# Performance work log

Measured on AMD Instinct MI355X. Metric: run time of the kernel, lower is better.

The kernel has to match this reference:

```python
import jax, jax.numpy as jnp
import numpy as np

N = 100000      # nodes
E = 1600000     # edges
F_IN, HID, OUT = 128, 64, 40


def gcn_conv(x, edge_index, W, b, num_nodes):
    """PyG GCNConv: linear transform, add self-loops, symmetric deg^-1/2 norm, scatter-add."""
    h = x @ W  # [N, F_out]
    loops = jnp.arange(num_nodes, dtype=edge_index.dtype)
    row = jnp.concatenate([edge_index[0], loops])  # source
    col = jnp.concatenate([edge_index[1], loops])  # target
    ones = jnp.ones(row.shape[0], dtype=h.dtype)
    deg = jax.ops.segment_sum(ones, col, num_segments=num_nodes)  # in-degree incl. self-loop
    dinv = jnp.where(deg > 0, jax.lax.rsqrt(deg), 0.0)
    norm = dinv[row] * dinv[col]                      # [E+N]
    msg = h[row] * norm[:, None]                      # gather + scale
    out = jax.ops.segment_sum(msg, col, num_segments=num_nodes)  # scatter-add
    return out + b


def setup_inputs() -> dict:
    key = jax.random.key(0)
    k = jax.random.split(key, 6)
    x = jax.random.normal(k[0], (N, F_IN), dtype=jnp.float32)
    edge_index = jax.random.randint(k[1], (2, E), 0, N, dtype=jnp.int32)
    W1 = jax.random.normal(k[2], (F_IN, HID), dtype=jnp.float32) / np.sqrt(F_IN)
    b1 = jnp.zeros((HID,), dtype=jnp.float32)
    W2 = jax.random.normal(k[3], (HID, OUT), dtype=jnp.float32) / np.sqrt(HID)
    b2 = jnp.zeros((OUT,), dtype=jnp.float32)
    return {"x": x, "edge_index": edge_index, "W1": W1, "b1": b1, "W2": W2, "b2": b2}


def reference(x, edge_index, W1, b1, W2, b2):
    h = gcn_conv(x, edge_index, W1, b1, N)
    h = jax.nn.relu(h)
    # dropout is identity in eval mode (F.dropout(training=False))
    h = gcn_conv(h, edge_index, W2, b2, N)
    return jax.nn.log_softmax(h, axis=1)
```

## Files before the change

kernel.cpp:

```cpp
#include <hip/hip_runtime.h>
#include <math.h>

#define NN 100000
#define NE 1600000
#define F_IN 128
#define HID 64
#define OUTF 40
#define NBKT 391
#define BCAPB 5120
#define TILE 16384
#define NTILES 98

typedef unsigned short u16;

__device__ __forceinline__ u16 f2bf(float f) {
    unsigned int x = __float_as_uint(f);
    return (u16)((x + 0x7fffu + ((x >> 16) & 1u)) >> 16);
}

__device__ __forceinline__ void add8(const int4 v, float* acc) {
    acc[0] += __uint_as_float(((unsigned)v.x) << 16);
    acc[1] += __uint_as_float(v.x & 0xffff0000u);
    acc[2] += __uint_as_float(((unsigned)v.y) << 16);
    acc[3] += __uint_as_float(v.y & 0xffff0000u);
    acc[4] += __uint_as_float(((unsigned)v.z) << 16);
    acc[5] += __uint_as_float(v.z & 0xffff0000u);
    acc[6] += __uint_as_float(((unsigned)v.w) << 16);
    acc[7] += __uint_as_float(v.w & 0xffff0000u);
}

__global__ void k_zero(int* bcnt) {
    int i = threadIdx.x;
    if (i < NBKT) bcnt[i] = 0;
}

__launch_bounds__(1024)
__global__ void k_bucket(const int* __restrict__ ei, int* __restrict__ bcnt,
                         int* __restrict__ bkt) {
    __shared__ int hist[NBKT], goff[NBKT], cur[NBKT];
    __shared__ int ss[512];
    __shared__ int stage[TILE];
    int t = threadIdx.x;
    int e0 = blockIdx.x * TILE;
    int ecnt = min(TILE, NE - e0);
    if (t < NBKT) hist[t] = 0;
    __syncthreads();
    for (int i = t; i < ecnt; i += 1024)
        atomicAdd(&hist[ei[NE + e0 + i] >> 8], 1);
    __syncthreads();
    if (t < 512) ss[t] = (t < NBKT) ? hist[t] : 0;
    __syncthreads();
    for (int o = 1; o < 512; o <<= 1) {
        int add = (t >= o && t < 512) ? ss[t - o] : 0;
        __syncthreads();
        if (t < 512) ss[t] += add;
        __syncthreads();
    }
    if (t < NBKT) cur[t] = ss[t] - hist[t];
    if (t < NBKT) goff[t] = atomicAdd(&bcnt[t], hist[t]);
    __syncthreads();
    for (int i = t; i < ecnt; i += 1024) {
        int c = ei[NE + e0 + i];
        int r = ei[e0 + i];
        int pos = atomicAdd(&cur[c >> 8], 1);
        stage[pos] = ((c & 255) << 17) | r;
    }
    __syncthreads();
    int wv = t >> 6, ln = t & 63;
    for (int b = wv; b < NBKT; b += 16) {
        int cnt = hist[b];
        int lo = cur[b] - cnt;
        int gb = b * BCAPB + goff[b];
        for (int i = ln; i < cnt; i += 64)
            bkt[gb + i] = stage[lo + i];
    }
}

__global__ void k_scanb(int* __restrict__ bcnt, int* __restrict__ bboff) {
    __shared__ int s[512];
    int t = threadIdx.x;
    int v = (t < NBKT) ? bcnt[t] : 0;
    s[t] = v;
    __syncthreads();
    for (int o = 1; o < 512; o <<= 1) {
        int add = (t >= o) ? s[t - o] : 0;
        __syncthreads();
        s[t] += add;
        __syncthreads();
    }
    if (t < NBKT) bboff[t] = s[t] - v;
}

__launch_bounds__(256)
__global__ void k_csr(const int* __restrict__ bcnt, const int* __restrict__ bboff,
                      const int* __restrict__ bkt, float* __restrict__ dinv,
                      int* __restrict__ cursor, int* __restrict__ eidx) {
    __shared__ int hist[256], loff[256], cur[256], sscan[256];
    __shared__ int stage[BCAPB];
    int t = threadIdx.x;
    int b = blockIdx.x;
    int cnt = bcnt[b];
    int base = bboff[b];
    const int* bp = bkt + b * BCAPB;
    hist[t] = 0;
    __syncthreads();
    for (int i = t; i < cnt; i += 256)
        atomicAdd(&hist[bp[i] >> 17], 1);
    __syncthreads();
    int n = b * 256 + t;
    int d = hist[t];
    if (n < NN) dinv[n] = rsqrtf((float)(d + 1));
    sscan[t] = d;
    __syncthreads();
    for (int o = 1; o < 256; o <<= 1) {
        int add = (t >= o) ? sscan[t - o] : 0;
        __syncthreads();
        sscan[t] += add;
        __syncthreads();
    }
    loff[t] = sscan[t] - d;
    cur[t] = 0;
    if (n < NN) cursor[n] = base + sscan[t];
    __syncthreads();
    for (int i = t; i < cnt; i += 256) {
        int v = bp[i];
        int pos = loff[v >> 17] + atomicAdd(&cur[v >> 17], 1);
        stage[pos] = v & 0x1FFFF;
    }
    __syncthreads();
    for (int i = t; i < cnt; i += 256)
        eidx[base + i] = stage[i];
}

__launch_bounds__(256)
__global__ void k_gemm1(const float* __restrict__ x, const float* __restrict__ W1,
                        const float* __restrict__ dinv, u16* __restrict__ h1) {
    __shared__ float Xs[64][132];
    __shared__ float Ws[128][64];
    int t = threadIdx.x;
    int row0 = blockIdx.x * 64;

#pragma unroll
    for (int i = 0; i < 8; i++) {
        int idx4 = t + 256 * i;
        float4 v = ((const float4*)W1)[idx4];
        int k = idx4 >> 4;
        int c4 = (idx4 & 15) << 2;
        *(float4*)&Ws[k][c4] = v;
    }
#pragma unroll
    for (int i = 0; i < 8; i++) {
        int idx4 = t + 256 * i;
        int r = idx4 >> 5;
        int k4 = (idx4 & 31) << 2;
        int gr = row0 + r;
        if (gr >= NN) gr = NN - 1;
        float4 v = *(const float4*)&x[gr * F_IN + k4];
        *(float4*)&Xs[r][k4] = v;
    }
    __syncthreads();

    int tx = t & 15, ty = t >> 4;
    int cb = tx << 2, rb = ty << 2;
    float acc[4][4] = {};
#pragma unroll 2
    for (int k = 0; k < F_IN; k += 4) {
        float4 xv[4], wv[4];
#pragma unroll
        for (int i = 0; i < 4; i++) xv[i] = *(const float4*)&Xs[rb + i][k];
#pragma unroll
        for (int kk = 0; kk < 4; kk++) wv[kk] = *(const float4*)&Ws[k + kk][cb];
#pragma unroll
        for (int i = 0; i < 4; i++) {
            const float* xp = (const float*)&xv[i];
#pragma unroll
            for (int kk = 0; kk < 4; kk++) {
                acc[i][0] += xp[kk] * wv[kk].x;
                acc[i][1] += xp[kk] * wv[kk].y;
                acc[i][2] += xp[kk] * wv[kk].z;
                acc[i][3] += xp[kk] * wv[kk].w;
            }
        }
    }
#pragma unroll
    for (int i = 0; i < 4; i++) {
        int gr = row0 + rb + i;
        if (gr < NN) {
            float dn = dinv[gr];
            ushort4 o;
            o.x = f2bf(acc[i][0] * dn); o.y = f2bf(acc[i][1] * dn);
            o.z = f2bf(acc[i][2] * dn); o.w = f2bf(acc[i][3] * dn);
            *(ushort4*)&h1[(size_t)gr * HID + cb] = o;
        }
    }
}

template <bool RELU_BIAS>
__global__ void k_agg(const int* __restrict__ cursor, const int* __restrict__ eidx,
                      const float* __restrict__ dinv, const u16* __restrict__ h,
                      const float* __restrict__ bias, u16* __restrict__ outp) {
    int lane = threadIdx.x & 63;
    int wid = (blockIdx.x * blockDim.x + threadIdx.x) >> 6;
    int half = lane >> 5;
    int li = lane & 31;
    int n = wid * 2 + half;
    int eg = (lane >> 3) & 3;
    int fo = (lane & 7) * 8;
    int hbase = lane & 32;
    int end = cursor[n];
    int start = (n == 0) ? 0 : cursor[n - 1];
    int deg = end - start;
    int degw = max(deg, __shfl_xor(deg, 32, 64));

    float acc[8] = {}, acc2[8] = {};
    if (eg == 0) {
        int4 hv = *(const int4*)&h[n * HID + fo];
        add8(hv, acc);
    }
    for (int c0 = 0; c0 < degw; c0 += 32) {
        int m = min(32, deg - c0);
        int mw = min(32, degw - c0);
        int sidx = (li < m) ? eidx[start + c0 + li] : 0;
        int kmax = (mw + 3) >> 2;
        int k = 0;
        for (; k + 2 <= kmax; k += 2) {
            int e0 = eg + (k << 2), e1 = e0 + 4;
            int s0 = __shfl(sidx, hbase + e0, 64);
            int s1 = __shfl(sidx, hbase + e1, 64);
            if (e0 < m) { int4 a = *(const int4*)&h[s0 * HID + fo]; add8(a, acc); }
            if (e1 < m) { int4 b = *(const int4*)&h[s1 * HID + fo]; add8(b, acc2); }
        }
        if (k < kmax) {
            int e0 = eg + (k << 2);
            int s0 = __shfl(sidx, hbase + e0, 64);
            if (e0 < m) { int4 a = *(const int4*)&h[s0 * HID + fo]; add8(a, acc); }
        }
    }
#pragma unroll
    for (int i = 0; i < 8; i++) acc[i] += acc2[i];

#pragma unroll
    for (int o = 8; o <= 16; o <<= 1) {
#pragma unroll
        for (int i = 0; i < 8; i++) acc[i] += __shfl_xor(acc[i], o, 64);
    }
    if (eg == 0) {
        float dn = dinv[n];
        if (RELU_BIAS) {
#pragma unroll
            for (int i = 0; i < 8; i++)
                acc[i] = fmaxf(dn * acc[i] + bias[fo + i], 0.f) * dn;
        } else {
#pragma unroll
            for (int i = 0; i < 8; i++) acc[i] *= dn;
        }
        int4 o;
        o.x = (int)f2bf(acc[0]) | ((int)f2bf(acc[1]) << 16);
        o.y = (int)f2bf(acc[2]) | ((int)f2bf(acc[3]) << 16);
        o.z = (int)f2bf(acc[4]) | ((int)f2bf(acc[5]) << 16);
        o.w = (int)f2bf(acc[6]) | ((int)f2bf(acc[7]) << 16);
        *(int4*)&outp[(size_t)n * HID + fo] = o;
    }
}

__launch_bounds__(320)
__global__ void k_gemm2(const u16* __restrict__ s_in, const float* __restrict__ W2,
                        const float* __restrict__ b2, float* __restrict__ outb) {
    __shared__ float As[128][68];
    __shared__ float Ws[64][40];
    __shared__ float rowm[128], rowls[128];
    int t = threadIdx.x;
    int row0 = blockIdx.x * 128;

    for (int i = t; i < 64 * 40; i += 320) Ws[i / 40][i % 40] = W2[i];

    for (int idx8 = t; idx8 < 1024; idx8 += 320) {
        int r = idx8 >> 3, k8 = (idx8 & 7) << 3;
        int gr = row0 + r;
        if (gr >= NN) gr = NN - 1;
        int4 v = *(const int4*)&s_in[(size_t)gr * HID + k8];
        float* dst = &As[r][k8];
        dst[0] = __uint_as_float(((unsigned)v.x) << 16);
        dst[1] = __uint_as_float(v.x & 0xffff0000u);
        dst[2] = __uint_as_float(((unsigned)v.y) << 16);
        dst[3] = __uint_as_float(v.y & 0xffff0000u);
        dst[4] = __uint_as_float(((unsigned)v.z) << 16);
        dst[5] = __uint_as_float(v.z & 0xffff0000u);
        dst[6] = __uint_as_float(((unsigned)v.w) << 16);
        dst[7] = __uint_as_float(v.w & 0xffff0000u);
    }
    __syncthreads();

    int tx = t % 10, ty = t / 10;
    int cb = tx * 4, rb = ty * 4;
    float acc[4][4] = {};
#pragma unroll 2
    for (int k = 0; k < HID; k += 4) {
        float4 xv[4], wv[4];
#pragma unroll
        for (int i = 0; i < 4; i++) xv[i] = *(const float4*)&As[rb + i][k];
#pragma unroll
        for (int kk = 0; kk < 4; kk++) wv[kk] = *(const float4*)&Ws[k + kk][cb];
#pragma unroll
        for (int i = 0; i < 4; i++) {
            const float* xp = (const float*)&xv[i];
#pragma unroll
            for (int kk = 0; kk < 4; kk++) {
                acc[i][0] += xp[kk] * wv[kk].x;
                acc[i][1] += xp[kk] * wv[kk].y;
                acc[i][2] += xp[kk] * wv[kk].z;
                acc[i][3] += xp[kk] * wv[kk].w;
            }
        }
    }
    float4 bb = *(const float4*)&b2[cb];
#pragma unroll
    for (int i = 0; i < 4; i++) {
        acc[i][0] += bb.x; acc[i][1] += bb.y;
        acc[i][2] += bb.z; acc[i][3] += bb.w;
    }

    __syncthreads();
    float* Os = &As[0][0];
#pragma unroll
    for (int i = 0; i < 4; i++) {
        int row = rb + i;
        Os[(cb + 0) * 132 + row] = acc[i][0];
        Os[(cb + 1) * 132 + row] = acc[i][1];
        Os[(cb + 2) * 132 + row] = acc[i][2];
        Os[(cb + 3) * 132 + row] = acc[i][3];
    }
    __syncthreads();
    if (t < 128) {
        float m = -INFINITY;
        for (int c = 0; c < OUTF; c++) m = fmaxf(m, Os[c * 132 + t]);
        float sum = 0.f;
        for (int c = 0; c < OUTF; c++) sum += __expf(Os[c * 132 + t] - m);
        rowm[t] = m;
        rowls[t] = __logf(sum);
    }
    __syncthreads();
#pragma unroll
    for (int i = 0; i < 4; i++) {
        int row = rb + i;
        int gr = row0 + row;
        if (gr < NN) {
            float sh = rowm[row] + rowls[row];
            *(float4*)&outb[(size_t)gr * OUTF + cb] =
                make_float4(acc[i][0] - sh, acc[i][1] - sh,
                            acc[i][2] - sh, acc[i][3] - sh);
        }
    }
}

extern "C" void kernel_launch(void* const* d_in, const int* in_sizes, int n_in,
                              void* d_out, int out_size, void* d_ws, size_t ws_size,
                              hipStream_t stream) {
    const float* x  = (const float*)d_in[0];
    const int*   ei = (const int*)d_in[1];
    const float* W1 = (const float*)d_in[2];
    const float* b1 = (const float*)d_in[3];
    const float* W2 = (const float*)d_in[4];
    const float* b2 = (const float*)d_in[5];
    float* outb = (float*)d_out;

    float* dinv   = (float*)d_ws;
    int*   cursor = (int*)d_ws + 100000;
    int*   bcnt   = (int*)d_ws + 200000;
    int*   bboff  = (int*)d_ws + 200512;
    int*   eidx   = (int*)d_ws + 201024;
    u16*   h1     = (u16*)((int*)d_ws + 1801024);
    u16*   r      = (u16*)((int*)d_ws + 5001024);
    u16*   s      = (u16*)((int*)d_ws + 8201024);
    int*   bkt    = (int*)s;

    k_zero<<<1, 512, 0, stream>>>(bcnt);
    k_bucket<<<NTILES, 1024, 0, stream>>>(ei, bcnt, bkt);
    k_scanb<<<1, 512, 0, stream>>>(bcnt, bboff);
    k_csr<<<NBKT, 256, 0, stream>>>(bcnt, bboff, bkt, dinv, cursor, eidx);

    k_gemm1<<<(NN + 63) / 64, 256, 0, stream>>>(x, W1, dinv, h1);
    k_agg<true><<<(NN / 2 * 64 + 255) / 256, 256, 0, stream>>>(cursor, eidx, dinv, h1, b1, r);
    k_agg<false><<<(NN / 2 * 64 + 255) / 256, 256, 0, stream>>>(cursor, eidx, dinv, r, nullptr, s);
    k_gemm2<<<(NN + 127) / 128, 320, 0, stream>>>(s, W2, b2, outb);
}
```

Measured before the change: 162.9 us.

## Use bf16 MFMA for first GEMM and halve bucket tile size

The first-layer GEMM now converts x and a transposed W1 to bf16 in shared memory and uses 16x16x32 bf16 MFMA instructions instead of scalar FP32 FMAs. The aim is to cut compute time and shared-memory footprint, at the cost of reduced input precision and scattered 2-byte output stores. Separately, the edge-bucketing kernel now uses 8192-edge tiles with 512 threads across twice as many blocks, for more parallelism and lower shared-memory use per block.

```diff
diff --git a/kernel.cpp b/kernel.cpp
--- a/kernel.cpp
+++ b/kernel.cpp
@@ -8,10 +8,12 @@
 #define OUTF 40
 #define NBKT 391
 #define BCAPB 5120
-#define TILE 16384
-#define NTILES 98
+#define TILE 8192
+#define NTILES 196
 
 typedef unsigned short u16;
+typedef __attribute__((ext_vector_type(8))) __bf16 bf16x8;
+typedef __attribute__((ext_vector_type(4))) float f32x4;
 
 __device__ __forceinline__ u16 f2bf(float f) {
     unsigned int x = __float_as_uint(f);
@@ -34,7 +36,7 @@
     if (i < NBKT) bcnt[i] = 0;
 }
 
-__launch_bounds__(1024)
+__launch_bounds__(512)
 __global__ void k_bucket(const int* __restrict__ ei, int* __restrict__ bcnt,
                          int* __restrict__ bkt) {
     __shared__ int hist[NBKT], goff[NBKT], cur[NBKT];
@@ -45,21 +47,21 @@
     int ecnt = min(TILE, NE - e0);
     if (t < NBKT) hist[t] = 0;
     __syncthreads();
-    for (int i = t; i < ecnt; i += 1024)
+    for (int i = t; i < ecnt; i += 512)
         atomicAdd(&hist[ei[NE + e0 + i] >> 8], 1);
     __syncthreads();
-    if (t < 512) ss[t] = (t < NBKT) ? hist[t] : 0;
+    ss[t] = (t < NBKT) ? hist[t] : 0;
     __syncthreads();
     for (int o = 1; o < 512; o <<= 1) {
-        int add = (t >= o && t < 512) ? ss[t - o] : 0;
-        __syncthreads();
-        if (t < 512) ss[t] += add;
+        int add = (t >= o) ? ss[t - o] : 0;
+        __syncthreads();
+        ss[t] += add;
         __syncthreads();
     }
     if (t < NBKT) cur[t] = ss[t] - hist[t];
     if (t < NBKT) goff[t] = atomicAdd(&bcnt[t], hist[t]);
     __syncthreads();
-    for (int i = t; i < ecnt; i += 1024) {
+    for (int i = t; i < ecnt; i += 512) {
         int c = ei[NE + e0 + i];
         int r = ei[e0 + i];
         int pos = atomicAdd(&cur[c >> 8], 1);
@@ -67,7 +69,7 @@
     }
     __syncthreads();
     int wv = t >> 6, ln = t & 63;
-    for (int b = wv; b < NBKT; b += 16) {
+    for (int b = wv; b < NBKT; b += 8) {
         int cnt = hist[b];
         int lo = cur[b] - cnt;
         int gb = b * BCAPB + goff[b];
@@ -135,62 +137,58 @@
 __launch_bounds__(256)
 __global__ void k_gemm1(const float* __restrict__ x, const float* __restrict__ W1,
                         const float* __restrict__ dinv, u16* __restrict__ h1) {
-    __shared__ float Xs[64][132];
-    __shared__ float Ws[128][64];
+    __shared__ u16 Xs[64][136];
+    __shared__ u16 Wt[64][136];
     int t = threadIdx.x;
     int row0 = blockIdx.x * 64;
 
-#pragma unroll
-    for (int i = 0; i < 8; i++) {
-        int idx4 = t + 256 * i;
-        float4 v = ((const float4*)W1)[idx4];
-        int k = idx4 >> 4;
-        int c4 = (idx4 & 15) << 2;
-        *(float4*)&Ws[k][c4] = v;
-    }
+    for (int idx = t; idx < F_IN * HID; idx += 256)
+        Wt[idx & 63][idx >> 6] = f2bf(W1[idx]);
 #pragma unroll
     for (int i = 0; i < 8; i++) {
         int idx4 = t + 256 * i;
         int r = idx4 >> 5;
-        int k4 = (idx4 & 31) << 2;
+        int c4 = (idx4 & 31) << 2;
         int gr = row0 + r;
         if (gr >= NN) gr = NN - 1;
-        float4 v = *(const float4*)&x[gr * F_IN + k4];
-        *(float4*)&Xs[r][k4] = v;
-    }
-    __syncthreads();
-
-    int tx = t & 15, ty = t >> 4;
-    int cb = tx << 2, rb = ty << 2;
-    float acc[4][4] = {};
-#pragma unroll 2
-    for (int k = 0; k < F_IN; k += 4) {
-        float4 xv[4], wv[4];
-#pragma unroll
-        for (int i = 0; i < 4; i++) xv[i] = *(const float4*)&Xs[rb + i][k];
-#pragma unroll
-        for (int kk = 0; kk < 4; kk++) wv[kk] = *(const float4*)&Ws[k + kk][cb];
-#pragma unroll
-        for (int i = 0; i < 4; i++) {
-            const float* xp = (const float*)&xv[i];
-#pragma unroll
-            for (int kk = 0; kk < 4; kk++) {
-                acc[i][0] += xp[kk] * wv[kk].x;
-                acc[i][1] += xp[kk] * wv[kk].y;
-                acc[i][2] += xp[kk] * wv[kk].z;
-                acc[i][3] += xp[kk] * wv[kk].w;
-            }
-        }
-    }
+        float4 v = *(const float4*)&x[gr * F_IN + c4];
+        ushort4 o;
+        o.x = f2bf(v.x); o.y = f2bf(v.y); o.z = f2bf(v.z); o.w = f2bf(v.w);
+        *(ushort4*)&Xs[r][c4] = o;
+    }
+    __syncthreads();
+
+    int wave = t >> 6, lane = t & 63;
+    int rloc = lane & 15;
+    int koct = (lane >> 4) * 8;
+    int wrow = wave * 16;
+
+    f32x4 acc0 = {}, acc1 = {}, acc2 = {}, acc3 = {};
+#pragma unroll
+    for (int s = 0; s < 4; s++) {
+        int k0 = s * 32 + koct;
+        bf16x8 a = *(const bf16x8*)&Xs[wrow + rloc][k0];
+        bf16x8 b0 = *(const bf16x8*)&Wt[rloc][k0];
+        bf16x8 b1 = *(const bf16x8*)&Wt[16 + rloc][k0];
+        bf16x8 b2 = *(const bf16x8*)&Wt[32 + rloc][k0];
+        bf16x8 b3 = *(const bf16x8*)&Wt[48 + rloc][k0];
+        acc0 = __builtin_amdgcn_mfma_f32_16x16x32_bf16(a, b0, acc0, 0, 0, 0);
+        acc1 = __builtin_amdgcn_mfma_f32_16x16x32_bf16(a, b1, acc1, 0, 0, 0);
+        acc2 = __builtin_amdgcn_mfma_f32_16x16x32_bf16(a, b2, acc2, 0, 0, 0);
+        acc3 = __builtin_amdgcn_mfma_f32_16x16x32_bf16(a, b3, acc3, 0, 0, 0);
+    }
+
+    int rq = (lane >> 4) * 4;
 #pragma unroll
     for (int i = 0; i < 4; i++) {
-        int gr = row0 + rb + i;
+        int gr = row0 + wrow + rq + i;
         if (gr < NN) {
             float dn = dinv[gr];
-            ushort4 o;
-            o.x = f2bf(acc[i][0] * dn); o.y = f2bf(acc[i][1] * dn);
-            o.z = f2bf(acc[i][2] * dn); o.w = f2bf(acc[i][3] * dn);
-            *(ushort4*)&h1[(size_t)gr * HID + cb] = o;
+            size_t base = (size_t)gr * HID + rloc;
+            h1[base]      = f2bf(acc0[i] * dn);
+            h1[base + 16] = f2bf(acc1[i] * dn);
+            h1[base + 32] = f2bf(acc2[i] * dn);
+            h1[base + 48] = f2bf(acc3[i] * dn);
         }
     }
 }
@@ -375,7 +373,7 @@
     int*   bkt    = (int*)s;
 
     k_zero<<<1, 512, 0, stream>>>(bcnt);
-    k_bucket<<<NTILES, 1024, 0, stream>>>(ei, bcnt, bkt);
+    k_bucket<<<NTILES, 512, 0, stream>>>(ei, bcnt, bkt);
     k_scanb<<<1, 512, 0, stream>>>(bcnt, bboff);
     k_csr<<<NBKT, 256, 0, stream>>>(bcnt, bboff, bkt, dinv, cursor, eidx);
 
```

New measurement: 155.0 us. 4.8% less time.
